# Performance work log

Measured on AMD Instinct MI355X. Metric: run time of the kernel, lower is better.

Reference implementation:

```python
import jax, jax.numpy as jnp
import numpy as np

B, V, T, D, H = 8, 64, 256, 256, 8
DH = D // H
LN_EPS = 1e-5


def setup_inputs() -> dict:
    key = jax.random.key(0)
    k0, k1, k2, k3 = jax.random.split(key, 4)
    x = jax.random.normal(k0, (B, V, T + 1, D), dtype=jnp.float32)
    obs_mask = jax.random.randint(k1, (B, V, T), 0, 2).astype(bool)
    ln_w = jnp.ones((D,), jnp.float32)
    ln_b = jnp.zeros((D,), jnp.float32)
    w_qkv = jax.random.normal(k2, (3 * D, D), dtype=jnp.float32) * 0.02   # torch Linear weight (out,in), no bias
    w_proj = jax.random.normal(k3, (D, D), dtype=jnp.float32) * 0.02
    b_proj = jnp.zeros((D,), jnp.float32)
    return dict(x=x, obs_mask=obs_mask, ln_w=ln_w, ln_b=ln_b,
                w_qkv=w_qkv, w_proj=w_proj, b_proj=b_proj)


def reference(x, obs_mask, ln_w, ln_b, w_qkv, w_proj, b_proj):
    b, v, t1, d = x.shape
    h, dh = H, D // H

    # LayerNorm over last dim
    mu = jnp.mean(x, axis=-1, keepdims=True)
    var = jnp.mean(jnp.square(x - mu), axis=-1, keepdims=True)
    xn = (x - mu) * jax.lax.rsqrt(var + LN_EPS) * ln_w + ln_b

    # QKV projection: (B,V,T1,3D) -> (B,V,T1,3,H,dh)
    qkv = jnp.einsum('bvtd,ed->bvte', xn, w_qkv).reshape(b, v, t1, 3, h, dh)
    qf = qkv[:, :, :, 0]  # (B,V,T1,H,dh)
    kf = qkv[:, :, :, 1]
    vf = qkv[:, :, :, 2]

    # Queries from position 0 only: (B,H,V,dh)
    q = jnp.transpose(qf[:, :, 0], (0, 2, 1, 3))

    # Keys: masked mean over time (query token at pos 0 always observed)
    mask = jnp.concatenate([jnp.ones((b, v, 1), bool), obs_mask], axis=2)  # (B,V,T1)
    mf = mask[..., None, None].astype(kf.dtype)                            # (B,V,T1,1,1)
    cnt = jnp.clip(mask.sum(axis=2).astype(kf.dtype), 1.0)[:, :, None, None]
    k = (kf * mf).sum(axis=2) / cnt                                        # (B,V,H,dh)
    k = jnp.transpose(k, (0, 2, 1, 3))                                     # (B,H,V,dh)

    # Small cross-variable attention matrix (B,H,V,V)
    scale = dh ** -0.5
    attn = jax.nn.softmax(jnp.einsum('bhqd,bhkd->bhqk', q, k) * scale, axis=-1)

    # Values packed with temporal structure: (B,H,V,dh,T1)
    vp = jnp.transpose(vf, (0, 3, 1, 4, 2))
    out = jnp.einsum('bhqk,bhkdt->bhqdt', attn, vp)                        # (B,H,V,dh,T1)

    # Unpack back to (B,V,T1,D)
    out = jnp.transpose(out, (0, 2, 4, 1, 3)).reshape(b, v, t1, d)
    out = out @ w_proj.T + b_proj
    return x + out
```

## Files before the change

kernel.cpp:

```cpp
#include <hip/hip_runtime.h>
#include <hip/hip_bf16.h>

typedef unsigned short u16;
typedef __attribute__((ext_vector_type(8))) short short8;
typedef __attribute__((ext_vector_type(4))) float f32x4;

#define B_ 8
#define V_ 64
#define T_ 256
#define T1_ 257
#define D_ 256
#define H_ 8
#define DH_ 32

__device__ __forceinline__ u16 f2bf(float f){
  union { float f; unsigned int u; } v; v.f = f;
  unsigned int u = v.u;
  return (u16)((u + 0x7fffu + ((u >> 16) & 1u)) >> 16);
}

__global__ void k0_conv(const float* __restrict__ wqkv, const float* __restrict__ wproj,
                        u16* __restrict__ wv, u16* __restrict__ wp, float* __restrict__ xsum){
  int i = blockIdx.x * 256 + threadIdx.x;
  if (i < 65536) wv[i] = f2bf(wqkv[131072 + i]);
  else           wp[i - 65536] = f2bf(wproj[i - 65536]);
  xsum[i] = 0.f;
}

__global__ void k1_ln(const float* __restrict__ x, const int* __restrict__ mask,
                      const float* __restrict__ lnw, const float* __restrict__ lnb,
                      float* __restrict__ musig, float* __restrict__ xsum){
  int bv = blockIdx.x;
  int tid = threadIdx.x;
  int lane = tid & 63, wid = tid >> 6;
  int half = lane >> 5, l32 = lane & 31;
  int c8 = l32 * 8;
  __shared__ float xsred[4][512];
  float4 w0 = *(const float4*)&lnw[c8], w1 = *(const float4*)&lnw[c8 + 4];
  float4 b0 = *(const float4*)&lnb[c8], b1 = *(const float4*)&lnb[c8 + 4];
  float xs[8];
  #pragma unroll
  for (int j = 0; j < 8; ++j) xs[j] = 0.f;
  for (int p = blockIdx.y * 4 + wid; p < 129; p += 16){
    int t = p * 2 + half;
    bool valid = (t < T1_);
    float4 a0 = {0.f,0.f,0.f,0.f}, a1 = {0.f,0.f,0.f,0.f};
    if (valid){
      const float* gp = &x[((long)bv * T1_ + t) * D_ + c8];
      a0 = *(const float4*)gp; a1 = *(const float4*)(gp + 4);
    }
    float s  = a0.x + a0.y + a0.z + a0.w + a1.x + a1.y + a1.z + a1.w;
    float s2 = a0.x*a0.x + a0.y*a0.y + a0.z*a0.z + a0.w*a0.w
             + a1.x*a1.x + a1.y*a1.y + a1.z*a1.z + a1.w*a1.w;
    #pragma unroll
    for (int off = 1; off < 32; off <<= 1){
      s  += __shfl_xor(s,  off, 64);
      s2 += __shfl_xor(s2, off, 64);
    }
    float mu   = s * (1.f / 256.f);
    float var  = s2 * (1.f / 256.f) - mu * mu;
    float rstd = rsqrtf(var + 1e-5f);
    if (valid){
      if (l32 == 0){
        musig[((long)bv * T1_ + t) * 2]     = mu;
        musig[((long)bv * T1_ + t) * 2 + 1] = rstd;
      }
      int m = (t == 0) ? 1 : mask[bv * T_ + (t - 1)];
      if (m){
        xs[0] += (a0.x - mu) * rstd * w0.x + b0.x;
        xs[1] += (a0.y - mu) * rstd * w0.y + b0.y;
        xs[2] += (a0.z - mu) * rstd * w0.z + b0.z;
        xs[3] += (a0.w - mu) * rstd * w0.w + b0.w;
        xs[4] += (a1.x - mu) * rstd * w1.x + b1.x;
        xs[5] += (a1.y - mu) * rstd * w1.y + b1.y;
        xs[6] += (a1.z - mu) * rstd * w1.z + b1.z;
        xs[7] += (a1.w - mu) * rstd * w1.w + b1.w;
      }
    }
  }
  #pragma unroll
  for (int j = 0; j < 8; ++j) xsred[wid][half * 256 + c8 + j] = xs[j];
  __syncthreads();
  float r = 0.f;
  #pragma unroll
  for (int w2 = 0; w2 < 4; ++w2) r += xsred[w2][tid] + xsred[w2][256 + tid];
  atomicAdd(&xsum[bv * D_ + tid], r);
}

__global__ void k2a_qk(const float* __restrict__ x, const int* __restrict__ mask,
                       const float* __restrict__ lnw, const float* __restrict__ lnb,
                       const float* __restrict__ wqkv,
                       const float* __restrict__ musig, const float* __restrict__ xsum,
                       float* __restrict__ qout, float* __restrict__ kout){
  int bv = blockIdx.x, tid = threadIdx.x;
  int lane = tid & 63, wid = tid >> 6;
  __shared__ __align__(16) float xn0[D_];
  __shared__ __align__(16) float xs[D_];
  __shared__ float redc[4];
  int s = mask[bv * T_ + tid];
  #pragma unroll
  for (int off = 32; off >= 1; off >>= 1) s += __shfl_down(s, off, 64);
  if (lane == 0) redc[wid] = (float)s;
  __syncthreads();
  float cnt = 1.f + redc[0] + redc[1] + redc[2] + redc[3];
  float mu = musig[((long)bv * T1_) * 2], rstd = musig[((long)bv * T1_) * 2 + 1];
  xn0[tid] = (x[((long)bv * T1_) * D_ + tid] - mu) * rstd * lnw[tid] + lnb[tid];
  xs[tid]  = xsum[bv * D_ + tid] * (1.f / cnt);
  __syncthreads();
  float4 xq = *(const float4*)&xn0[lane * 4];
  float4 xk = *(const float4*)&xs[lane * 4];
  int e0 = (blockIdx.y * 4 + wid) * 16;
  for (int i = 0; i < 16; ++i){
    int e = e0 + i;
    float4 wq4 = *(const float4*)&wqkv[(long)e * D_ + lane * 4];
    float4 wk4 = *(const float4*)&wqkv[(long)(256 + e) * D_ + lane * 4];
    float sq = xq.x*wq4.x + xq.y*wq4.y + xq.z*wq4.z + xq.w*wq4.w;
    float sk = xk.x*wk4.x + xk.y*wk4.y + xk.z*wk4.z + xk.w*wk4.w;
    #pragma unroll
    for (int off = 32; off >= 1; off >>= 1){
      sq += __shfl_down(sq, off, 64);
      sk += __shfl_down(sk, off, 64);
    }
    if (lane == 0){ qout[bv * D_ + e] = sq; kout[bv * D_ + e] = sk; }
  }
}

__global__ void k2b_attn(const float* __restrict__ q, const float* __restrict__ k,
                         u16* __restrict__ attn){
  int bh = blockIdx.x; int b = bh >> 3, h = bh & 7;
  int tid = threadIdx.x;
  int lane = tid & 63, wid = tid >> 6;
  __shared__ float qs[64][33], ks[64][33];
  #pragma unroll
  for (int j = 0; j < 2; ++j){
    int i4 = tid * 2 + j;
    int r = i4 >> 3, c4 = (i4 & 7) * 4;
    float4 vq = *(const float4*)&q[((long)(b * V_ + r)) * D_ + h * DH_ + c4];
    float4 vk = *(const float4*)&k[((long)(b * V_ + r)) * D_ + h * DH_ + c4];
    qs[r][c4] = vq.x; qs[r][c4+1] = vq.y; qs[r][c4+2] = vq.z; qs[r][c4+3] = vq.w;
    ks[r][c4] = vk.x; ks[r][c4+1] = vk.y; ks[r][c4+2] = vk.z; ks[r][c4+3] = vk.w;
  }
  __syncthreads();
  const float scale = 0.17677669529663687f;
  for (int i = 0; i < 16; ++i){
    int qr = i * 4 + wid;
    float a = 0.f;
    #pragma unroll
    for (int d = 0; d < DH_; ++d) a += qs[qr][d] * ks[lane][d];
    a *= scale;
    float mx = a;
    #pragma unroll
    for (int off = 1; off < 64; off <<= 1) mx = fmaxf(mx, __shfl_xor(mx, off, 64));
    float e = __expf(a - mx);
    float sum = e;
    #pragma unroll
    for (int off = 1; off < 64; off <<= 1) sum += __shfl_xor(sum, off, 64);
    attn[((long)bh * 64 + qr) * 64 + lane] = f2bf(e * (1.f / sum));
  }
}

__global__ __launch_bounds__(512, 4) void k3_main(
    const float* __restrict__ x, const float* __restrict__ lnw, const float* __restrict__ lnb,
    const float* __restrict__ bproj, const float* __restrict__ musig,
    const u16* __restrict__ wv, const u16* __restrict__ wp,
    const u16* __restrict__ attn, float* __restrict__ out){
  constexpr int XS = 264;
  constexpr int VS = 72;
  __shared__ __align__(16) u16 Xs[64 * XS];
  __shared__ __align__(16) u16 VT[D_ * VS];
  __shared__ float lnw_s[D_], lnb_s[D_], bp_s[D_];
  __shared__ float ms_s[V_ * 2];

  int bt = blockIdx.x; int b = bt / T1_, t = bt % T1_;
  int tid = threadIdx.x;
  int w = tid >> 6, lane = tid & 63, lm = lane & 15, lq = lane >> 4;
  int cw = w * 32;
  int h = w;

  short8 wvf[16];
  #pragma unroll
  for (int kk = 0; kk < 8; ++kk)
    #pragma unroll
    for (int nt = 0; nt < 2; ++nt)
      wvf[kk*2+nt] = *(const short8*)&wv[(long)(cw + nt*16 + lm) * D_ + kk*32 + lq*8];

  float4 xa[8];
  #pragma unroll
  for (int i = 0; i < 4; ++i){
    int seg = i * 512 + tid;
    int vr = seg >> 5;
    int c8 = (seg & 31) * 8;
    const float* gp = x + (((long)b * V_ + vr) * T1_ + t) * D_ + c8;
    xa[i*2]   = *(const float4*)gp;
    xa[i*2+1] = *(const float4*)(gp + 4);
  }

  if (tid < 256){ lnw_s[tid] = lnw[tid]; lnb_s[tid] = lnb[tid]; bp_s[tid] = bproj[tid]; }
  else if (tid < 384){
    int i = tid - 256;
    ms_s[i] = musig[(((long)b * V_ + (i >> 1)) * T1_ + t) * 2 + (i & 1)];
  }
  __syncthreads();

  #pragma unroll
  for (int i = 0; i < 4; ++i){
    int seg = i * 512 + tid;
    int vr = seg >> 5;
    int c8 = (seg & 31) * 8;
    float mu = ms_s[vr * 2], rs = ms_s[vr * 2 + 1];
    float av[8] = {xa[i*2].x, xa[i*2].y, xa[i*2].z, xa[i*2].w,
                   xa[i*2+1].x, xa[i*2+1].y, xa[i*2+1].z, xa[i*2+1].w};
    union { u16 us[8]; uint4 q4; } pk;
    #pragma unroll
    for (int j = 0; j < 8; ++j)
      pk.us[j] = f2bf((av[j] - mu) * rs * lnw_s[c8 + j] + lnb_s[c8 + j]);
    *(uint4*)&Xs[vr * XS + c8] = pk.q4;
  }
  __syncthreads();

  f32x4 acc1[4][2];
  #pragma unroll
  for (int mt = 0; mt < 4; ++mt)
    #pragma unroll
    for (int nt = 0; nt < 2; ++nt) acc1[mt][nt] = (f32x4){0.f, 0.f, 0.f, 0.f};
  #pragma unroll
  for (int kk = 0; kk < 8; ++kk){
    short8 af[4];
    #pragma unroll
    for (int mt = 0; mt < 4; ++mt)
      af[mt] = *(const short8*)&Xs[(mt * 16 + lm) * XS + kk * 32 + lq * 8];
    #pragma unroll
    for (int mt = 0; mt < 4; ++mt)
      #pragma unroll
      for (int nt = 0; nt < 2; ++nt)
        acc1[mt][nt] = __builtin_amdgcn_mfma_f32_16x16x32_bf16(af[mt], wvf[kk*2+nt], acc1[mt][nt], 0, 0, 0);
  }
  #pragma unroll
  for (int mt = 0; mt < 4; ++mt)
    #pragma unroll
    for (int nt = 0; nt < 2; ++nt){
      int col = cw + nt * 16 + lm;
      int row = mt * 16 + lq * 4;
      union { u16 us[4]; uint2 q2; } pv;
      #pragma unroll
      for (int r = 0; r < 4; ++r) pv.us[r] = f2bf(acc1[mt][nt][r]);
      *(uint2*)&VT[col * VS + row] = pv.q2;
    }

  short8 atf[8];
  #pragma unroll
  for (int kk = 0; kk < 2; ++kk)
    #pragma unroll
    for (int mt = 0; mt < 4; ++mt)
      atf[kk*4+mt] = *(const short8*)&attn[((long)(b * H_ + h) * 64 + mt * 16 + lm) * 64 + kk * 32 + lq * 8];
  short8 wpf0[8];
  #pragma unroll
  for (int kk = 0; kk < 4; ++kk)
    #pragma unroll
    for (int nt = 0; nt < 2; ++nt)
      wpf0[kk*2+nt] = *(const short8*)&wp[(long)(cw + nt*16 + lm) * D_ + kk*32 + lq*8];
  __syncthreads();

  f32x4 acc2[4][2];
  #pragma unroll
  for (int mt = 0; mt < 4; ++mt)
    #pragma unroll
    for (int nt = 0; nt < 2; ++nt) acc2[mt][nt] = (f32x4){0.f, 0.f, 0.f, 0.f};
  #pragma unroll
  for (int kk = 0; kk < 2; ++kk){
    short8 bfr[2];
    #pragma unroll
    for (int nt = 0; nt < 2; ++nt)
      bfr[nt] = *(const short8*)&VT[(h * 32 + nt * 16 + lm) * VS + kk * 32 + lq * 8];
    #pragma unroll
    for (int mt = 0; mt < 4; ++mt)
      #pragma unroll
      for (int nt = 0; nt < 2; ++nt)
        acc2[mt][nt] = __builtin_amdgcn_mfma_f32_16x16x32_bf16(atf[kk*4+mt], bfr[nt], acc2[mt][nt], 0, 0, 0);
  }
  short8 wpf1[8];
  #pragma unroll
  for (int kk = 0; kk < 4; ++kk)
    #pragma unroll
    for (int nt = 0; nt < 2; ++nt)
      wpf1[kk*2+nt] = *(const short8*)&wp[(long)(cw + nt*16 + lm) * D_ + (kk + 4)*32 + lq*8];
  #pragma unroll
  for (int mt = 0; mt < 4; ++mt)
    #pragma unroll
    for (int nt = 0; nt < 2; ++nt){
      int col = h * 32 + nt * 16 + lm;
      #pragma unroll
      for (int r = 0; r < 4; ++r){
        int row = mt * 16 + lq * 4 + r;
        Xs[row * XS + col] = f2bf(acc2[mt][nt][r]);
      }
    }
  __syncthreads();

  f32x4 acc3[4][2];
  #pragma unroll
  for (int mt = 0; mt < 4; ++mt)
    #pragma unroll
    for (int nt = 0; nt < 2; ++nt) acc3[mt][nt] = (f32x4){0.f, 0.f, 0.f, 0.f};
  #pragma unroll
  for (int kk = 0; kk < 4; ++kk){
    short8 af[4];
    #pragma unroll
    for (int mt = 0; mt < 4; ++mt)
      af[mt] = *(const short8*)&Xs[(mt * 16 + lm) * XS + kk * 32 + lq * 8];
    #pragma unroll
    for (int mt = 0; mt < 4; ++mt)
      #pragma unroll
      for (int nt = 0; nt < 2; ++nt)
        acc3[mt][nt] = __builtin_amdgcn_mfma_f32_16x16x32_bf16(af[mt], wpf0[kk*2+nt], acc3[mt][nt], 0, 0, 0);
  }
  #pragma unroll
  for (int kk = 0; kk < 4; ++kk){
    short8 af[4];
    #pragma unroll
    for (int mt = 0; mt < 4; ++mt)
      af[mt] = *(const short8*)&Xs[(mt * 16 + lm) * XS + (kk + 4) * 32 + lq * 8];
    #pragma unroll
    for (int mt = 0; mt < 4; ++mt)
      #pragma unroll
      for (int nt = 0; nt < 2; ++nt)
        acc3[mt][nt] = __builtin_amdgcn_mfma_f32_16x16x32_bf16(af[mt], wpf1[kk*2+nt], acc3[mt][nt], 0, 0, 0);
  }
  float rx[4][2][4];
  #pragma unroll
  for (int mt = 0; mt < 4; ++mt)
    #pragma unroll
    for (int nt = 0; nt < 2; ++nt){
      int e = cw + nt * 16 + lm;
      #pragma unroll
      for (int r = 0; r < 4; ++r){
        int vr = mt * 16 + lq * 4 + r;
        rx[mt][nt][r] = x[(((long)b * V_ + vr) * T1_ + t) * D_ + e];
      }
    }
  #pragma unroll
  for (int mt = 0; mt < 4; ++mt)
    #pragma unroll
    for (int nt = 0; nt < 2; ++nt){
      int e = cw + nt * 16 + lm;
      #pragma unroll
      for (int r = 0; r < 4; ++r){
        int vr = mt * 16 + lq * 4 + r;
        long g = (((long)b * V_ + vr) * T1_ + t) * D_ + e;
        out[g] = acc3[mt][nt][r] + bp_s[e] + rx[mt][nt][r];
      }
    }
}

extern "C" void kernel_launch(void* const* d_in, const int* in_sizes, int n_in,
                              void* d_out, int out_size, void* d_ws, size_t ws_size,
                              hipStream_t stream){
  const float* x     = (const float*)d_in[0];
  const int*   mask  = (const int*)d_in[1];
  const float* lnw   = (const float*)d_in[2];
  const float* lnb   = (const float*)d_in[3];
  const float* wqkv  = (const float*)d_in[4];
  const float* wproj = (const float*)d_in[5];
  const float* bproj = (const float*)d_in[6];
  float* out = (float*)d_out;
  char* ws = (char*)d_ws;
  float* musig = (float*)(ws);
  float* xsum  = (float*)(ws + 1052672);
  float* qbuf  = (float*)(ws + 1576960);
  float* kbuf  = (float*)(ws + 2101248);
  u16*   attn  = (u16*)  (ws + 2625536);
  u16*   wv    = (u16*)  (ws + 3149824);
  u16*   wp    = (u16*)  (ws + 3280896);

  k0_conv<<<512, 256, 0, stream>>>(wqkv, wproj, wv, wp, xsum);
  k1_ln<<<dim3(512, 4), 256, 0, stream>>>(x, mask, lnw, lnb, musig, xsum);
  k2a_qk<<<dim3(512, 4), 256, 0, stream>>>(x, mask, lnw, lnb, wqkv, musig, xsum, qbuf, kbuf);
  k2b_attn<<<64, 256, 0, stream>>>(qbuf, kbuf, attn);
  k3_main<<<B_ * T1_, 512, 0, stream>>>(x, lnw, lnb, bproj, musig, wv, wp, attn, out);
}
```

Baseline: 383.2 us.

## Fuse weight conversion into LN kernel, drop VT smem via shuffles, raise occupancy

The bf16 weight conversion moves into extra blocks of the LN kernel, and that kernel now uses 512 threads per (b,v) with a direct store, so the zeroing pass and atomics go away. The attention-softmax kernel is split across a second grid dimension for more blocks. In the main kernel, the V-projection result no longer goes through the VT shared buffer; it is passed between lanes with cross-lane shuffles. Weight fragments are streamed per k-step instead of being preloaded into registers. Together these cut shared memory and register use so launch_bounds can ask for 6 blocks, at the cost of more global weight reloads and shuffle instructions.

```diff
diff --git a/kernel.cpp b/kernel.cpp
--- a/kernel.cpp
+++ b/kernel.cpp
@@ -19,29 +19,29 @@
   return (u16)((u + 0x7fffu + ((u >> 16) & 1u)) >> 16);
 }
 
-__global__ void k0_conv(const float* __restrict__ wqkv, const float* __restrict__ wproj,
-                        u16* __restrict__ wv, u16* __restrict__ wp, float* __restrict__ xsum){
-  int i = blockIdx.x * 256 + threadIdx.x;
-  if (i < 65536) wv[i] = f2bf(wqkv[131072 + i]);
-  else           wp[i - 65536] = f2bf(wproj[i - 65536]);
-  xsum[i] = 0.f;
-}
-
 __global__ void k1_ln(const float* __restrict__ x, const int* __restrict__ mask,
                       const float* __restrict__ lnw, const float* __restrict__ lnb,
-                      float* __restrict__ musig, float* __restrict__ xsum){
+                      const float* __restrict__ wqkv, const float* __restrict__ wproj,
+                      float* __restrict__ musig, float* __restrict__ xsum,
+                      u16* __restrict__ wv, u16* __restrict__ wp){
+  if (blockIdx.x >= 512){
+    int j = (blockIdx.x - 512) * 512 + threadIdx.x;
+    wv[j] = f2bf(wqkv[131072 + j]);
+    wp[j] = f2bf(wproj[j]);
+    return;
+  }
   int bv = blockIdx.x;
   int tid = threadIdx.x;
   int lane = tid & 63, wid = tid >> 6;
   int half = lane >> 5, l32 = lane & 31;
   int c8 = l32 * 8;
-  __shared__ float xsred[4][512];
+  __shared__ float xsred[8][512];
   float4 w0 = *(const float4*)&lnw[c8], w1 = *(const float4*)&lnw[c8 + 4];
   float4 b0 = *(const float4*)&lnb[c8], b1 = *(const float4*)&lnb[c8 + 4];
   float xs[8];
   #pragma unroll
   for (int j = 0; j < 8; ++j) xs[j] = 0.f;
-  for (int p = blockIdx.y * 4 + wid; p < 129; p += 16){
+  for (int p = wid; p < 129; p += 8){
     int t = p * 2 + half;
     bool valid = (t < T1_);
     float4 a0 = {0.f,0.f,0.f,0.f}, a1 = {0.f,0.f,0.f,0.f};
@@ -81,10 +81,12 @@
   #pragma unroll
   for (int j = 0; j < 8; ++j) xsred[wid][half * 256 + c8 + j] = xs[j];
   __syncthreads();
-  float r = 0.f;
-  #pragma unroll
-  for (int w2 = 0; w2 < 4; ++w2) r += xsred[w2][tid] + xsred[w2][256 + tid];
-  atomicAdd(&xsum[bv * D_ + tid], r);
+  if (tid < 256){
+    float r = 0.f;
+    #pragma unroll
+    for (int w2 = 0; w2 < 8; ++w2) r += xsred[w2][tid] + xsred[w2][256 + tid];
+    xsum[bv * D_ + tid] = r;
+  }
 }
 
 __global__ void k2a_qk(const float* __restrict__ x, const int* __restrict__ mask,
@@ -142,7 +144,7 @@
   }
   __syncthreads();
   const float scale = 0.17677669529663687f;
-  for (int i = 0; i < 16; ++i){
+  for (int i = blockIdx.y * 4; i < blockIdx.y * 4 + 4; ++i){
     int qr = i * 4 + wid;
     float a = 0.f;
     #pragma unroll
@@ -159,15 +161,13 @@
   }
 }
 
-__global__ __launch_bounds__(512, 4) void k3_main(
+__global__ __launch_bounds__(512, 6) void k3_main(
     const float* __restrict__ x, const float* __restrict__ lnw, const float* __restrict__ lnb,
     const float* __restrict__ bproj, const float* __restrict__ musig,
     const u16* __restrict__ wv, const u16* __restrict__ wp,
     const u16* __restrict__ attn, float* __restrict__ out){
   constexpr int XS = 264;
-  constexpr int VS = 72;
   __shared__ __align__(16) u16 Xs[64 * XS];
-  __shared__ __align__(16) u16 VT[D_ * VS];
   __shared__ float lnw_s[D_], lnb_s[D_], bp_s[D_];
   __shared__ float ms_s[V_ * 2];
 
@@ -177,39 +177,23 @@
   int cw = w * 32;
   int h = w;
 
-  short8 wvf[16];
-  #pragma unroll
-  for (int kk = 0; kk < 8; ++kk)
-    #pragma unroll
-    for (int nt = 0; nt < 2; ++nt)
-      wvf[kk*2+nt] = *(const short8*)&wv[(long)(cw + nt*16 + lm) * D_ + kk*32 + lq*8];
-
-  float4 xa[8];
+  if (tid < 256){ lnw_s[tid] = lnw[tid]; lnb_s[tid] = lnb[tid]; bp_s[tid] = bproj[tid]; }
+  else if (tid < 384){
+    int i = tid - 256;
+    ms_s[i] = musig[(((long)b * V_ + (i >> 1)) * T1_ + t) * 2 + (i & 1)];
+  }
+  __syncthreads();
+
   #pragma unroll
   for (int i = 0; i < 4; ++i){
     int seg = i * 512 + tid;
     int vr = seg >> 5;
     int c8 = (seg & 31) * 8;
     const float* gp = x + (((long)b * V_ + vr) * T1_ + t) * D_ + c8;
-    xa[i*2]   = *(const float4*)gp;
-    xa[i*2+1] = *(const float4*)(gp + 4);
-  }
-
-  if (tid < 256){ lnw_s[tid] = lnw[tid]; lnb_s[tid] = lnb[tid]; bp_s[tid] = bproj[tid]; }
-  else if (tid < 384){
-    int i = tid - 256;
-    ms_s[i] = musig[(((long)b * V_ + (i >> 1)) * T1_ + t) * 2 + (i & 1)];
-  }
-  __syncthreads();
-
-  #pragma unroll
-  for (int i = 0; i < 4; ++i){
-    int seg = i * 512 + tid;
-    int vr = seg >> 5;
-    int c8 = (seg & 31) * 8;
+    float4 a0 = *(const float4*)gp;
+    float4 a1 = *(const float4*)(gp + 4);
     float mu = ms_s[vr * 2], rs = ms_s[vr * 2 + 1];
-    float av[8] = {xa[i*2].x, xa[i*2].y, xa[i*2].z, xa[i*2].w,
-                   xa[i*2+1].x, xa[i*2+1].y, xa[i*2+1].z, xa[i*2+1].w};
+    float av[8] = {a0.x, a0.y, a0.z, a0.w, a1.x, a1.y, a1.z, a1.w};
     union { u16 us[8]; uint4 q4; } pk;
     #pragma unroll
     for (int j = 0; j < 8; ++j)
@@ -223,67 +207,63 @@
   for (int mt = 0; mt < 4; ++mt)
     #pragma unroll
     for (int nt = 0; nt < 2; ++nt) acc1[mt][nt] = (f32x4){0.f, 0.f, 0.f, 0.f};
-  #pragma unroll
   for (int kk = 0; kk < 8; ++kk){
-    short8 af[4];
+    short8 af[4], bfr[2];
     #pragma unroll
     for (int mt = 0; mt < 4; ++mt)
       af[mt] = *(const short8*)&Xs[(mt * 16 + lm) * XS + kk * 32 + lq * 8];
     #pragma unroll
+    for (int nt = 0; nt < 2; ++nt)
+      bfr[nt] = *(const short8*)&wv[(long)(cw + nt * 16 + lm) * D_ + kk * 32 + lq * 8];
+    #pragma unroll
     for (int mt = 0; mt < 4; ++mt)
       #pragma unroll
       for (int nt = 0; nt < 2; ++nt)
-        acc1[mt][nt] = __builtin_amdgcn_mfma_f32_16x16x32_bf16(af[mt], wvf[kk*2+nt], acc1[mt][nt], 0, 0, 0);
-  }
-  #pragma unroll
-  for (int mt = 0; mt < 4; ++mt)
+        acc1[mt][nt] = __builtin_amdgcn_mfma_f32_16x16x32_bf16(af[mt], bfr[nt], acc1[mt][nt], 0, 0, 0);
+  }
+
+  unsigned int pw[4][2][2];
+  #pragma unroll
+  for (int mt = 0; mt < 4; ++mt)
+    #pragma unroll
+    for (int nt = 0; nt < 2; ++nt)
+      #pragma unroll
+      for (int p = 0; p < 2; ++p)
+        pw[mt][nt][p] = (unsigned int)f2bf(acc1[mt][nt][2*p])
+                      | ((unsigned int)f2bf(acc1[mt][nt][2*p+1]) << 16);
+
+  f32x4 acc2[4][2];
+  #pragma unroll
+  for (int mt = 0; mt < 4; ++mt)
+    #pragma unroll
+    for (int nt = 0; nt < 2; ++nt) acc2[mt][nt] = (f32x4){0.f, 0.f, 0.f, 0.f};
+  #pragma unroll
+  for (int kk = 0; kk < 2; ++kk){
+    short8 bfrm[2];
     #pragma unroll
     for (int nt = 0; nt < 2; ++nt){
-      int col = cw + nt * 16 + lm;
-      int row = mt * 16 + lq * 4;
-      union { u16 us[4]; uint2 q2; } pv;
-      #pragma unroll
-      for (int r = 0; r < 4; ++r) pv.us[r] = f2bf(acc1[mt][nt][r]);
-      *(uint2*)&VT[col * VS + row] = pv.q2;
-    }
-
-  short8 atf[8];
-  #pragma unroll
-  for (int kk = 0; kk < 2; ++kk)
-    #pragma unroll
-    for (int mt = 0; mt < 4; ++mt)
-      atf[kk*4+mt] = *(const short8*)&attn[((long)(b * H_ + h) * 64 + mt * 16 + lm) * 64 + kk * 32 + lq * 8];
-  short8 wpf0[8];
-  #pragma unroll
-  for (int kk = 0; kk < 4; ++kk)
-    #pragma unroll
-    for (int nt = 0; nt < 2; ++nt)
-      wpf0[kk*2+nt] = *(const short8*)&wp[(long)(cw + nt*16 + lm) * D_ + kk*32 + lq*8];
-  __syncthreads();
-
-  f32x4 acc2[4][2];
-  #pragma unroll
-  for (int mt = 0; mt < 4; ++mt)
-    #pragma unroll
-    for (int nt = 0; nt < 2; ++nt) acc2[mt][nt] = (f32x4){0.f, 0.f, 0.f, 0.f};
-  #pragma unroll
-  for (int kk = 0; kk < 2; ++kk){
-    short8 bfr[2];
-    #pragma unroll
-    for (int nt = 0; nt < 2; ++nt)
-      bfr[nt] = *(const short8*)&VT[(h * 32 + nt * 16 + lm) * VS + kk * 32 + lq * 8];
+      union { unsigned int wq[4]; short8 s8; } u;
+      #pragma unroll
+      for (int j2 = 0; j2 < 4; ++j2){
+        int srcLane = ((lq & 1) * 2 + (j2 >> 1)) * 16 + lm;
+        unsigned int va = __shfl((int)pw[2*kk    ][nt][j2 & 1], srcLane, 64);
+        unsigned int vb = __shfl((int)pw[2*kk + 1][nt][j2 & 1], srcLane, 64);
+        u.wq[j2] = (lq >= 2) ? vb : va;
+      }
+      bfrm[nt] = u.s8;
+    }
+    short8 atf[4];
+    #pragma unroll
+    for (int mt = 0; mt < 4; ++mt)
+      atf[mt] = *(const short8*)&attn[((long)(b * H_ + h) * 64 + mt * 16 + lm) * 64 + kk * 32 + lq * 8];
     #pragma unroll
     for (int mt = 0; mt < 4; ++mt)
       #pragma unroll
       for (int nt = 0; nt < 2; ++nt)
-        acc2[mt][nt] = __builtin_amdgcn_mfma_f32_16x16x32_bf16(atf[kk*4+mt], bfr[nt], acc2[mt][nt], 0, 0, 0);
-  }
-  short8 wpf1[8];
-  #pragma unroll
-  for (int kk = 0; kk < 4; ++kk)
-    #pragma unroll
-    for (int nt = 0; nt < 2; ++nt)
-      wpf1[kk*2+nt] = *(const short8*)&wp[(long)(cw + nt*16 + lm) * D_ + (kk + 4)*32 + lq*8];
+        acc2[mt][nt] = __builtin_amdgcn_mfma_f32_16x16x32_bf16(atf[mt], bfrm[nt], acc2[mt][nt], 0, 0, 0);
+  }
+  __syncthreads();
+
   #pragma unroll
   for (int mt = 0; mt < 4; ++mt)
     #pragma unroll
@@ -302,42 +282,20 @@
   for (int mt = 0; mt < 4; ++mt)
     #pragma unroll
     for (int nt = 0; nt < 2; ++nt) acc3[mt][nt] = (f32x4){0.f, 0.f, 0.f, 0.f};
-  #pragma unroll
-  for (int kk = 0; kk < 4; ++kk){
-    short8 af[4];
+  for (int kk = 0; kk < 8; ++kk){
+    short8 af[4], bfr[2];
     #pragma unroll
     for (int mt = 0; mt < 4; ++mt)
       af[mt] = *(const short8*)&Xs[(mt * 16 + lm) * XS + kk * 32 + lq * 8];
     #pragma unroll
+    for (int nt = 0; nt < 2; ++nt)
+      bfr[nt] = *(const short8*)&wp[(long)(cw + nt * 16 + lm) * D_ + kk * 32 + lq * 8];
+    #pragma unroll
     for (int mt = 0; mt < 4; ++mt)
       #pragma unroll
       for (int nt = 0; nt < 2; ++nt)
-        acc3[mt][nt] = __builtin_amdgcn_mfma_f32_16x16x32_bf16(af[mt], wpf0[kk*2+nt], acc3[mt][nt], 0, 0, 0);
-  }
-  #pragma unroll
-  for (int kk = 0; kk < 4; ++kk){
-    short8 af[4];
-    #pragma unroll
-    for (int mt = 0; mt < 4; ++mt)
-      af[mt] = *(const short8*)&Xs[(mt * 16 + lm) * XS + (kk + 4) * 32 + lq * 8];
-    #pragma unroll
-    for (int mt = 0; mt < 4; ++mt)
-      #pragma unroll
-      for (int nt = 0; nt < 2; ++nt)
-        acc3[mt][nt] = __builtin_amdgcn_mfma_f32_16x16x32_bf16(af[mt], wpf1[kk*2+nt], acc3[mt][nt], 0, 0, 0);
-  }
-  float rx[4][2][4];
-  #pragma unroll
-  for (int mt = 0; mt < 4; ++mt)
-    #pragma unroll
-    for (int nt = 0; nt < 2; ++nt){
-      int e = cw + nt * 16 + lm;
-      #pragma unroll
-      for (int r = 0; r < 4; ++r){
-        int vr = mt * 16 + lq * 4 + r;
-        rx[mt][nt][r] = x[(((long)b * V_ + vr) * T1_ + t) * D_ + e];
-      }
-    }
+        acc3[mt][nt] = __builtin_amdgcn_mfma_f32_16x16x32_bf16(af[mt], bfr[nt], acc3[mt][nt], 0, 0, 0);
+  }
   #pragma unroll
   for (int mt = 0; mt < 4; ++mt)
     #pragma unroll
@@ -347,7 +305,7 @@
       for (int r = 0; r < 4; ++r){
         int vr = mt * 16 + lq * 4 + r;
         long g = (((long)b * V_ + vr) * T1_ + t) * D_ + e;
-        out[g] = acc3[mt][nt][r] + bp_s[e] + rx[mt][nt][r];
+        out[g] = acc3[mt][nt][r] + bp_s[e] + x[g];
       }
     }
 }
@@ -372,9 +330,8 @@
   u16*   wv    = (u16*)  (ws + 3149824);
   u16*   wp    = (u16*)  (ws + 3280896);
 
-  k0_conv<<<512, 256, 0, stream>>>(wqkv, wproj, wv, wp, xsum);
-  k1_ln<<<dim3(512, 4), 256, 0, stream>>>(x, mask, lnw, lnb, musig, xsum);
+  k1_ln<<<640, 512, 0, stream>>>(x, mask, lnw, lnb, wqkv, wproj, musig, xsum, wv, wp);
   k2a_qk<<<dim3(512, 4), 256, 0, stream>>>(x, mask, lnw, lnb, wqkv, musig, xsum, qbuf, kbuf);
-  k2b_attn<<<64, 256, 0, stream>>>(qbuf, kbuf, attn);
+  k2b_attn<<<dim3(64, 4), 256, 0, stream>>>(qbuf, kbuf, attn);
   k3_main<<<B_ * T1_, 512, 0, stream>>>(x, lnw, lnb, bproj, musig, wv, wp, attn, out);
 }
```

Measured after the change: 406.0 us. 1.06x slower.
